# Kernel tuning notes

Measured on AMD Instinct MI355X. Metric: run time of the kernel, lower is better.

## Reference

```python
import jax, jax.numpy as jnp
import numpy as np

EPS = 1e-12
NUM_ITERATIONS = 3


def squash(t, axis=-1):
    sn = jnp.sum(t * t, axis=axis, keepdims=True)
    scale = sn / (1.0 + sn + EPS)
    return scale * t / jnp.sqrt(sn + EPS)


def setup_inputs() -> dict:
    key = jax.random.key(0)
    k1, k2 = jax.random.split(key)
    B, R, IN, OUT, C = 128, 4096, 16, 32, 2
    x = jax.random.normal(k1, (B, R, IN), dtype=jnp.float32)
    # learned parameter: torch.randn(num_capsules, num_route_nodes, in, out)
    route_weights = jax.random.normal(k2, (C, R, IN, OUT), dtype=jnp.float32)
    return {"x": x, "route_weights": route_weights}


def reference(x, route_weights):
    # priors: [C, B, R, 1, O] == x[None,:,:,None,:] @ W[:,None,:,:,:]
    priors = jnp.einsum('bri,crio->cbro', x, route_weights)[..., None, :]
    # logits kept [C,B,R,1,1]: the torch code stores [C,B,R,1,O] but every
    # update (delta_logits) is constant along O, so softmax over axis=2 is identical.
    logits = jnp.zeros(priors.shape[:-1] + (1,), dtype=priors.dtype)
    outputs = None
    for i in range(NUM_ITERATIONS):
        probs = jax.nn.softmax(logits, axis=2)                      # over route nodes
        s = jnp.sum(probs * priors, axis=2, keepdims=True)          # [C,B,1,1,O]
        outputs = squash(s, axis=-1)
        if i != NUM_ITERATIONS - 1:
            delta = jnp.sum(priors * outputs, axis=-1, keepdims=True)  # [C,B,R,1,1]
            logits = logits + delta
    return outputs
```

## Files before the change

kernel.cpp:

```cpp
#include <hip/hip_runtime.h>
#include <math.h>

#define CB    128
#define CR    4096
#define CIN   16
#define COUT  32
#define CCAP  2
#define RC    16
#define NRCH  (CR / RC)
#define EPSF  1e-12f

typedef _Float16 h8  __attribute__((ext_vector_type(8)));
typedef _Float16 h4t __attribute__((ext_vector_type(4)));
typedef float    f4  __attribute__((ext_vector_type(4)));

__global__ __launch_bounds__(512) void caps_pass_kernel(
    const float* __restrict__ x, const float* __restrict__ w,
    const float* __restrict__ vsum,
    float* __restrict__ partialA, float* __restrict__ partialE,
    int uniform)
{
  const int blk = (int)blockIdx.x;
  const int c   = blk >> 8;
  const int rch = blk & 255;
  const int r0  = rch * RC;
  const int t   = (int)threadIdx.x;
  const int wv  = t >> 6;
  const int L   = t & 63;
  const int g   = L >> 4;
  const int m   = L & 15;
  const int b   = wv * 16 + m;

  __shared__ __align__(16) char lds[36864];
  float*    Wst = (float*)lds;
  _Float16* WpL = (_Float16*)lds;
  float (*OutL)[40] = (float (*)[40])(lds + 16384);

  {
    const float4* src = (const float4*)(w + ((size_t)c * CR + r0) * 512);
#pragma unroll
    for (int k = 0; k < 4; ++k) ((float4*)Wst)[t + k * 512] = src[t + k * 512];
  }
  __syncthreads();

  h4t pk[4];
#pragma unroll
  for (int q = 0; q < 4; ++q) {
    const int sl  = t * 4 + q;
    const int rr  = sl >> 7;
    const int rem = sl & 127;
    const int ot  = rem >> 6;
    const int Ls  = rem & 63;
    const int gs  = Ls >> 4, ms = Ls & 15;
#pragma unroll
    for (int j = 0; j < 4; ++j)
      pk[q][j] = (_Float16)Wst[rr * 512 + (4 * gs + j) * 32 + ot * 16 + ms];
  }
  __syncthreads();
#pragma unroll
  for (int q = 0; q < 4; ++q) ((h4t*)WpL)[t * 4 + q] = pk[q];

  float4 vA = {0.f, 0.f, 0.f, 0.f}, vB = {0.f, 0.f, 0.f, 0.f};
  if (!uniform) {
    const float* vb = vsum + ((size_t)c * CB + b) * COUT;
    vA = *(const float4*)(vb + 4 * g);
    vB = *(const float4*)(vb + 16 + 4 * g);
  }

  float accA[4] = {0.f, 0.f, 0.f, 0.f};
  float accB[4] = {0.f, 0.f, 0.f, 0.f};
  float esum = 0.f;

  __syncthreads();

#pragma unroll 4
  for (int ri = 0; ri < RC; ++ri) {
    const int r = r0 + ri;
    float4 xf = *(const float4*)(x + ((size_t)b * CR + r) * CIN + 4 * g);
    h8 bx = {(_Float16)xf.x, (_Float16)xf.y, (_Float16)xf.z, (_Float16)xf.w,
             (_Float16)0.f, (_Float16)0.f, (_Float16)0.f, (_Float16)0.f};
    h4t wA4 = *(const h4t*)(WpL + ri * 512 + L * 4);
    h4t wB4 = *(const h4t*)(WpL + ri * 512 + 256 + L * 4);
    h8 aA = {wA4[0], wA4[1], wA4[2], wA4[3],
             (_Float16)0.f, (_Float16)0.f, (_Float16)0.f, (_Float16)0.f};
    h8 aB = {wB4[0], wB4[1], wB4[2], wB4[3],
             (_Float16)0.f, (_Float16)0.f, (_Float16)0.f, (_Float16)0.f};
    f4 z = {0.f, 0.f, 0.f, 0.f};
    f4 pA = __builtin_amdgcn_mfma_f32_16x16x32_f16(aA, bx, z, 0, 0, 0);
    f4 pB = __builtin_amdgcn_mfma_f32_16x16x32_f16(aB, bx, z, 0, 0, 0);

    float e;
    if (uniform) {
      e = 1.f;
    } else {
      float d = pA[0] * vA.x + pA[1] * vA.y + pA[2] * vA.z + pA[3] * vA.w
              + pB[0] * vB.x + pB[1] * vB.y + pB[2] * vB.z + pB[3] * vB.w;
      d += __shfl_xor(d, 16);
      d += __shfl_xor(d, 32);
      e = __expf(d);
    }
    esum += e;
#pragma unroll
    for (int j = 0; j < 4; ++j) { accA[j] += e * pA[j]; accB[j] += e * pB[j]; }
  }

#pragma unroll
  for (int j = 0; j < 4; ++j) {
    OutL[b][4 * g + j]      = accA[j];
    OutL[b][16 + 4 * g + j] = accB[j];
  }
  if (g == 0) OutL[b][32] = esum;
  __syncthreads();

  {
    const int bb = t >> 2, q = t & 3;
    float4 v0 = *(const float4*)&OutL[bb][q * 8];
    float4 v1 = *(const float4*)&OutL[bb][q * 8 + 4];
    float* dst = partialA + (((size_t)(c * NRCH + rch)) * CB + bb) * COUT + q * 8;
    *(float4*)dst = v0;
    *(float4*)(dst + 4) = v1;
    if (t < 128) partialE[((size_t)(c * NRCH + rch)) * CB + t] = OutL[t][32];
  }
}

__global__ __launch_bounds__(256) void caps_redv_kernel(
    const float* __restrict__ partialA, const float* __restrict__ partialE,
    float* __restrict__ vsum, float* __restrict__ out, int mode)
{
  const int cb = (int)blockIdx.x;
  const int c  = cb >> 7, b = cb & 127;
  const int t  = (int)threadIdx.x;
  const int o  = t & 31, jg = t >> 5;

  __shared__ float red[8][33];
  __shared__ float rede[8];

  float s = 0.f;
#pragma unroll 4
  for (int k = 0; k < 32; ++k) {
    const int j = jg + k * 8;
    s += partialA[(((size_t)(c * NRCH + j)) * CB + b) * COUT + o];
  }
  red[jg][o] = s;
  __syncthreads();

  if (t < 8) {
    float e = 0.f;
#pragma unroll 4
    for (int k = 0; k < 32; ++k)
      e += partialE[((size_t)(c * NRCH + t + k * 8)) * CB + b];
    rede[t] = e;
  }
  __syncthreads();

  if (t < 32) {
    float sv = red[0][t] + red[1][t] + red[2][t] + red[3][t] +
               red[4][t] + red[5][t] + red[6][t] + red[7][t];
    float es = rede[0] + rede[1] + rede[2] + rede[3] +
               rede[4] + rede[5] + rede[6] + rede[7];
    float sm = sv / es;
    float sn = sm * sm;
#pragma unroll
    for (int sh = 1; sh < 32; sh <<= 1) sn += __shfl_xor(sn, sh);
    float fac = sn / ((1.f + sn + EPSF) * sqrtf(sn + EPSF));
    float vv = sm * fac;
    if (mode == 2)      out[cb * COUT + t]  = vv;
    else if (mode == 1) vsum[cb * COUT + t] += vv;
    else                vsum[cb * COUT + t] = vv;
  }
}

extern "C" void kernel_launch(void* const* d_in, const int* in_sizes, int n_in,
                              void* d_out, int out_size, void* d_ws, size_t ws_size,
                              hipStream_t stream) {
  const float* x = (const float*)d_in[0];
  const float* w = (const float*)d_in[1];
  float* out = (float*)d_out;

  char* p = (char*)d_ws;
  float* vsum = (float*)p;
  p += (size_t)CCAP * CB * COUT * sizeof(float);
  float* partialA = (float*)p;
  p += (size_t)CCAP * NRCH * CB * COUT * sizeof(float);
  float* partialE = (float*)p;

  for (int it = 0; it < 3; ++it) {
    caps_pass_kernel<<<dim3(CCAP * NRCH), 512, 0, stream>>>(
        x, w, vsum, partialA, partialE, it == 0 ? 1 : 0);
    caps_redv_kernel<<<dim3(CCAP * CB), 256, 0, stream>>>(
        partialA, partialE, vsum, out, it == 0 ? 0 : (it == 1 ? 1 : 2));
  }
}
```

Baseline: 71.65 us.

## Fuse routing iterations into one cooperative kernel with grid syncs

Replaces the six alternating pass/reduce launches with a single cooperative kernel of 512 blocks. Each block stages and packs its fp16 weight chunk into LDS once and reuses it across all three routing iterations, using grid.sync between the pass and reduce phases. Partial sums are now written directly from registers in MFMA fragment order, which drops the LDS transpose, and the reducer uses matching indexing. This is meant to cut launch gaps and repeated weight loads and conversion, at the cost of grid-wide barriers, and it falls back to the multi-launch path if the cooperative launch is unavailable.

```diff
diff --git a/kernel.cpp b/kernel.cpp
--- a/kernel.cpp
+++ b/kernel.cpp
@@ -1,5 +1,8 @@
 #include <hip/hip_runtime.h>
+#include <hip/hip_cooperative_groups.h>
 #include <math.h>
+
+namespace cg = cooperative_groups;
 
 #define CB    128
 #define CR    4096
@@ -8,57 +11,53 @@
 #define CCAP  2
 #define RC    16
 #define NRCH  (CR / RC)
+#define GRID  (CCAP * NRCH)
 #define EPSF  1e-12f
 
 typedef _Float16 h8  __attribute__((ext_vector_type(8)));
 typedef _Float16 h4t __attribute__((ext_vector_type(4)));
 typedef float    f4  __attribute__((ext_vector_type(4)));
 
-__global__ __launch_bounds__(512) void caps_pass_kernel(
-    const float* __restrict__ x, const float* __restrict__ w,
-    const float* __restrict__ vsum,
-    float* __restrict__ partialA, float* __restrict__ partialE,
-    int uniform)
-{
-  const int blk = (int)blockIdx.x;
-  const int c   = blk >> 8;
-  const int rch = blk & 255;
-  const int r0  = rch * RC;
-  const int t   = (int)threadIdx.x;
-  const int wv  = t >> 6;
-  const int L   = t & 63;
-  const int g   = L >> 4;
-  const int m   = L & 15;
-  const int b   = wv * 16 + m;
-
-  __shared__ __align__(16) char lds[36864];
-  float*    Wst = (float*)lds;
-  _Float16* WpL = (_Float16*)lds;
-  float (*OutL)[40] = (float (*)[40])(lds + 16384);
-
-  {
-    const float4* src = (const float4*)(w + ((size_t)c * CR + r0) * 512);
-#pragma unroll
-    for (int k = 0; k < 4; ++k) ((float4*)Wst)[t + k * 512] = src[t + k * 512];
-  }
-  __syncthreads();
-
-  h4t pk[4];
-#pragma unroll
-  for (int q = 0; q < 4; ++q) {
-    const int sl  = t * 4 + q;
-    const int rr  = sl >> 7;
-    const int rem = sl & 127;
-    const int ot  = rem >> 6;
-    const int Ls  = rem & 63;
-    const int gs  = Ls >> 4, ms = Ls & 15;
-#pragma unroll
-    for (int j = 0; j < 4; ++j)
-      pk[q][j] = (_Float16)Wst[rr * 512 + (4 * gs + j) * 32 + ot * 16 + ms];
-  }
-  __syncthreads();
-#pragma unroll
-  for (int q = 0; q < 4; ++q) ((h4t*)WpL)[t * 4 + q] = pk[q];
+__device__ __forceinline__ void stage_pack_W(const float* __restrict__ w,
+                                             int c, int r0, int t,
+                                             _Float16* WpL, float* Stg)
+{
+  h4t* WpL4 = (h4t*)WpL;
+#pragma unroll
+  for (int h = 0; h < 2; ++h) {
+    const float4* src = (const float4*)(w + ((size_t)c * CR + r0 + h * 8) * 512);
+    ((float4*)Stg)[t]       = src[t];
+    ((float4*)Stg)[t + 512] = src[t + 512];
+    __syncthreads();
+#pragma unroll
+    for (int q = 0; q < 2; ++q) {
+      const int sl  = t * 2 + q;
+      const int rr  = sl >> 7;
+      const int rem = sl & 127;
+      const int ot  = rem >> 6;
+      const int gs  = (rem >> 4) & 3;
+      const int ms  = rem & 15;
+      h4t v;
+#pragma unroll
+      for (int j = 0; j < 4; ++j)
+        v[j] = (_Float16)Stg[rr * 512 + (4 * gs + j) * 32 + ot * 16 + ms];
+      WpL4[(h * 8 + rr) * 128 + rem] = v;
+    }
+    __syncthreads();
+  }
+}
+
+__device__ __forceinline__ void pass_body(const float* __restrict__ x,
+                                          const float* __restrict__ vsum,
+                                          float* __restrict__ partialA,
+                                          float* __restrict__ partialE,
+                                          const _Float16* WpL,
+                                          int c, int rch, int t, int uniform)
+{
+  const int r0 = rch * RC;
+  const int wv = t >> 6, L = t & 63, g = L >> 4, m = L & 15;
+  const int b  = wv * 16 + m;
+  const h4t* WpL4 = (const h4t*)WpL;
 
   float4 vA = {0.f, 0.f, 0.f, 0.f}, vB = {0.f, 0.f, 0.f, 0.f};
   if (!uniform) {
@@ -66,12 +65,9 @@
     vA = *(const float4*)(vb + 4 * g);
     vB = *(const float4*)(vb + 16 + 4 * g);
   }
-
   float accA[4] = {0.f, 0.f, 0.f, 0.f};
   float accB[4] = {0.f, 0.f, 0.f, 0.f};
   float esum = 0.f;
-
-  __syncthreads();
 
 #pragma unroll 4
   for (int ri = 0; ri < RC; ++ri) {
@@ -79,8 +75,8 @@
     float4 xf = *(const float4*)(x + ((size_t)b * CR + r) * CIN + 4 * g);
     h8 bx = {(_Float16)xf.x, (_Float16)xf.y, (_Float16)xf.z, (_Float16)xf.w,
              (_Float16)0.f, (_Float16)0.f, (_Float16)0.f, (_Float16)0.f};
-    h4t wA4 = *(const h4t*)(WpL + ri * 512 + L * 4);
-    h4t wB4 = *(const h4t*)(WpL + ri * 512 + 256 + L * 4);
+    h4t wA4 = WpL4[ri * 128 + L];
+    h4t wB4 = WpL4[ri * 128 + 64 + L];
     h8 aA = {wA4[0], wA4[1], wA4[2], wA4[3],
              (_Float16)0.f, (_Float16)0.f, (_Float16)0.f, (_Float16)0.f};
     h8 aB = {wB4[0], wB4[1], wB4[2], wB4[3],
@@ -89,10 +85,8 @@
     f4 pA = __builtin_amdgcn_mfma_f32_16x16x32_f16(aA, bx, z, 0, 0, 0);
     f4 pB = __builtin_amdgcn_mfma_f32_16x16x32_f16(aB, bx, z, 0, 0, 0);
 
-    float e;
-    if (uniform) {
-      e = 1.f;
-    } else {
+    float e = 1.f;
+    if (!uniform) {
       float d = pA[0] * vA.x + pA[1] * vA.y + pA[2] * vA.z + pA[3] * vA.w
               + pB[0] * vB.x + pB[1] * vB.y + pB[2] * vB.z + pB[3] * vB.w;
       d += __shfl_xor(d, 16);
@@ -104,60 +98,50 @@
     for (int j = 0; j < 4; ++j) { accA[j] += e * pA[j]; accB[j] += e * pB[j]; }
   }
 
-#pragma unroll
-  for (int j = 0; j < 4; ++j) {
-    OutL[b][4 * g + j]      = accA[j];
-    OutL[b][16 + 4 * g + j] = accB[j];
-  }
-  if (g == 0) OutL[b][32] = esum;
-  __syncthreads();
-
-  {
-    const int bb = t >> 2, q = t & 3;
-    float4 v0 = *(const float4*)&OutL[bb][q * 8];
-    float4 v1 = *(const float4*)&OutL[bb][q * 8 + 4];
-    float* dst = partialA + (((size_t)(c * NRCH + rch)) * CB + bb) * COUT + q * 8;
-    *(float4*)dst = v0;
-    *(float4*)(dst + 4) = v1;
-    if (t < 128) partialE[((size_t)(c * NRCH + rch)) * CB + t] = OutL[t][32];
-  }
-}
-
-__global__ __launch_bounds__(256) void caps_redv_kernel(
-    const float* __restrict__ partialA, const float* __restrict__ partialE,
-    float* __restrict__ vsum, float* __restrict__ out, int mode)
-{
-  const int cb = (int)blockIdx.x;
-  const int c  = cb >> 7, b = cb & 127;
-  const int t  = (int)threadIdx.x;
-  const int o  = t & 31, jg = t >> 5;
-
-  __shared__ float red[8][33];
-  __shared__ float rede[8];
+  float4 a4 = {accA[0], accA[1], accA[2], accA[3]};
+  float4 b4 = {accB[0], accB[1], accB[2], accB[3]};
+  float* dst = partialA + ((size_t)(c * NRCH + rch)) * 4096 + (size_t)t * 8;
+  *(float4*)dst = a4;
+  *(float4*)(dst + 4) = b4;
+  if (g == 0) partialE[((size_t)(c * NRCH + rch)) * CB + b] = esum;
+}
+
+template <int JG>
+__device__ __forceinline__ void redv_body(const float* __restrict__ partialA,
+                                          const float* __restrict__ partialE,
+                                          float* __restrict__ vsum,
+                                          float* __restrict__ out,
+                                          float (*red)[33], float* rede,
+                                          int cb, int t, int mode)
+{
+  const int c2 = cb >> 7, b2 = cb & 127;
+  const int o = t & 31, jg = t >> 5;
+  const int wv2 = b2 >> 4, m2 = b2 & 15;
+  const int half = o >> 4, oo = o & 15, g2 = oo >> 2, j2 = oo & 3;
+  const size_t idx = (size_t)(wv2 * 64 + g2 * 16 + m2) * 8 + half * 4 + j2;
 
   float s = 0.f;
 #pragma unroll 4
-  for (int k = 0; k < 32; ++k) {
-    const int j = jg + k * 8;
-    s += partialA[(((size_t)(c * NRCH + j)) * CB + b) * COUT + o];
+  for (int k = 0; k < NRCH / JG; ++k) {
+    const int j = jg + k * JG;
+    s += partialA[((size_t)(c2 * NRCH + j)) * 4096 + idx];
   }
   red[jg][o] = s;
   __syncthreads();
 
-  if (t < 8) {
+  if (t < JG) {
     float e = 0.f;
 #pragma unroll 4
-    for (int k = 0; k < 32; ++k)
-      e += partialE[((size_t)(c * NRCH + t + k * 8)) * CB + b];
+    for (int k = 0; k < NRCH / JG; ++k)
+      e += partialE[((size_t)(c2 * NRCH + t + k * JG)) * CB + b2];
     rede[t] = e;
   }
   __syncthreads();
 
   if (t < 32) {
-    float sv = red[0][t] + red[1][t] + red[2][t] + red[3][t] +
-               red[4][t] + red[5][t] + red[6][t] + red[7][t];
-    float es = rede[0] + rede[1] + rede[2] + rede[3] +
-               rede[4] + rede[5] + rede[6] + rede[7];
+    float sv = 0.f, es = 0.f;
+#pragma unroll
+    for (int jj = 0; jj < JG; ++jj) { sv += red[jj][t]; es += rede[jj]; }
     float sm = sv / es;
     float sn = sm * sm;
 #pragma unroll
@@ -170,6 +154,63 @@
   }
 }
 
+__global__ __launch_bounds__(512, 4) void caps_coop_kernel(
+    const float* __restrict__ x, const float* __restrict__ w,
+    float* __restrict__ vsum, float* __restrict__ partialA,
+    float* __restrict__ partialE, float* __restrict__ out)
+{
+  cg::grid_group grid = cg::this_grid();
+  const int blk = (int)blockIdx.x;
+  const int c = blk >> 8, rch = blk & 255;
+  const int t = (int)threadIdx.x;
+
+  __shared__ __align__(16) char lds[32768];
+  _Float16* WpL = (_Float16*)lds;
+  float* Stg = (float*)(lds + 16384);
+  float (*red)[33] = (float (*)[33])(lds + 16384);
+  float* rede = (float*)(lds + 16384 + 16 * 33 * 4);
+
+  stage_pack_W(w, c, rch * RC, t, WpL, Stg);
+
+#pragma unroll 1
+  for (int it = 0; it < 3; ++it) {
+    pass_body(x, vsum, partialA, partialE, WpL, c, rch, t, it == 0);
+    __threadfence();
+    grid.sync();
+    if (blk < 256)
+      redv_body<16>(partialA, partialE, vsum, out, red, rede, blk, t, it);
+    if (it < 2) {
+      __threadfence();
+      grid.sync();
+    }
+  }
+}
+
+__global__ __launch_bounds__(512) void caps_pass_kernel(
+    const float* __restrict__ x, const float* __restrict__ w,
+    const float* __restrict__ vsum, float* __restrict__ partialA,
+    float* __restrict__ partialE, int uniform)
+{
+  const int blk = (int)blockIdx.x;
+  const int c = blk >> 8, rch = blk & 255;
+  const int t = (int)threadIdx.x;
+  __shared__ __align__(16) char lds[32768];
+  _Float16* WpL = (_Float16*)lds;
+  float* Stg = (float*)(lds + 16384);
+  stage_pack_W(w, c, rch * RC, t, WpL, Stg);
+  pass_body(x, vsum, partialA, partialE, WpL, c, rch, t, uniform);
+}
+
+__global__ __launch_bounds__(256) void caps_redv_kernel(
+    const float* __restrict__ partialA, const float* __restrict__ partialE,
+    float* __restrict__ vsum, float* __restrict__ out, int mode)
+{
+  __shared__ float red[8][33];
+  __shared__ float rede[8];
+  redv_body<8>(partialA, partialE, vsum, out, red, rede,
+               (int)blockIdx.x, (int)threadIdx.x, mode);
+}
+
 extern "C" void kernel_launch(void* const* d_in, const int* in_sizes, int n_in,
                               void* d_out, int out_size, void* d_ws, size_t ws_size,
                               hipStream_t stream) {
@@ -181,13 +222,29 @@
   float* vsum = (float*)p;
   p += (size_t)CCAP * CB * COUT * sizeof(float);
   float* partialA = (float*)p;
-  p += (size_t)CCAP * NRCH * CB * COUT * sizeof(float);
+  p += (size_t)CCAP * NRCH * 4096 * sizeof(float);
   float* partialE = (float*)p;
 
+  int maxB = 0;
+  bool coop_ok =
+      (hipOccupancyMaxActiveBlocksPerMultiprocessor(
+           &maxB, (const void*)caps_coop_kernel, 512, 0) == hipSuccess) &&
+      (maxB >= 2);
+
+  if (coop_ok) {
+    void* args[] = {(void*)&x, (void*)&w, (void*)&vsum,
+                    (void*)&partialA, (void*)&partialE, (void*)&out};
+    hipError_t e = hipLaunchCooperativeKernel((const void*)caps_coop_kernel,
+                                              dim3(GRID), dim3(512), args, 0,
+                                              stream);
+    if (e == hipSuccess) return;
+    (void)hipGetLastError();
+  }
+
   for (int it = 0; it < 3; ++it) {
-    caps_pass_kernel<<<dim3(CCAP * NRCH), 512, 0, stream>>>(
+    caps_pass_kernel<<<dim3(GRID), 512, 0, stream>>>(
         x, w, vsum, partialA, partialE, it == 0 ? 1 : 0);
     caps_redv_kernel<<<dim3(CCAP * CB), 256, 0, stream>>>(
-        partialA, partialE, vsum, out, it == 0 ? 0 : (it == 1 ? 1 : 2));
-  }
-}
+        partialA, partialE, vsum, out, it);
+  }
+}
```

Result: slower. 75.92 us (+6.0%).
